# Performance work log

Measured on AMD Instinct MI355X. Metric: run time of the kernel, lower is better.

Reference implementation:

```python
import jax, jax.numpy as jnp
import numpy as np

N_SKILLS = 50000
N_EDGES = 800000
EMB = 128
HEADS = 2
HEAD_DIM = EMB // HEADS  # 64
N_LAYERS = 2
NEG_SLOPE = 0.2  # PyG GATv2Conv default negative_slope


def setup_inputs() -> dict:
    key = jax.random.key(0)
    ks = jax.random.split(key, 10)
    # Random edges with no self loops (PyG remove_self_loops is then a no-op).
    src = jax.random.randint(ks[0], (N_EDGES,), 0, N_SKILLS)
    off = jax.random.randint(ks[1], (N_EDGES,), 1, N_SKILLS)
    dst = (src + off) % N_SKILLS
    edge_index = jnp.stack([src, dst]).astype(jnp.int64)
    edge_weight = jax.random.uniform(ks[2], (N_EDGES,), dtype=jnp.float32)
    scale = 1.0 / np.sqrt(EMB)
    emb = jax.random.normal(ks[3], (N_SKILLS, EMB), dtype=jnp.float32)
    Wl = jax.random.normal(ks[4], (N_LAYERS, EMB, EMB), dtype=jnp.float32) * scale  # lin_l (source)
    Wr = jax.random.normal(ks[5], (N_LAYERS, EMB, EMB), dtype=jnp.float32) * scale  # lin_r (target)
    We = jax.random.normal(ks[6], (N_LAYERS, 1, EMB), dtype=jnp.float32)            # lin_edge
    att = jax.random.normal(ks[7], (N_LAYERS, HEADS, HEAD_DIM), dtype=jnp.float32) * (1.0 / np.sqrt(HEAD_DIM))
    bias = jnp.zeros((N_LAYERS, EMB), dtype=jnp.float32)
    return {"edge_index": edge_index, "edge_weight": edge_weight, "emb": emb,
            "Wl": Wl, "Wr": Wr, "We": We, "att": att, "bias": bias}


def _gatv2_layer(h, src, dst, ew, Wl, Wr, We, att, bias):
    """One GATv2Conv layer (concat heads, add_self_loops with fill_value='mean')."""
    N = h.shape[0]
    xl = (h @ Wl).reshape(N, HEADS, HEAD_DIM)  # source transform
    xr = (h @ Wr).reshape(N, HEADS, HEAD_DIM)  # target transform
    # Self-loop edge attr = mean of incoming edge attrs (PyG fill_value='mean').
    deg = jnp.zeros((N,), h.dtype).at[dst].add(1.0)
    loop_w = jnp.zeros((N,), h.dtype).at[dst].add(ew) / jnp.maximum(deg, 1.0)
    ar = jnp.arange(N)
    srcA = jnp.concatenate([src, ar])
    dstA = jnp.concatenate([dst, ar])
    ewA = jnp.concatenate([ew, loop_w])[:, None]           # [E+N, 1]
    e_emb = (ewA @ We).reshape(-1, HEADS, HEAD_DIM)        # [E+N, H, D]
    msg = xl[srcA]                                         # gathered source feats
    x = jax.nn.leaky_relu(msg + xr[dstA] + e_emb, NEG_SLOPE)
    alpha = jnp.einsum('ehd,hd->eh', x, att)               # [E+N, H]
    # Scatter-softmax over edges grouped by target node.
    amax = jnp.full((N, HEADS), -jnp.inf, h.dtype).at[dstA].max(alpha)
    ex = jnp.exp(alpha - amax[dstA])
    denom = jnp.zeros((N, HEADS), h.dtype).at[dstA].add(ex)
    a = ex / denom[dstA]                                   # denom > 0 (self loops)
    out = jnp.zeros((N, HEADS, HEAD_DIM), h.dtype).at[dstA].add(msg * a[:, :, None])
    return out.reshape(N, EMB) + bias


def reference(edge_index, edge_weight, emb, Wl, Wr, We, att, bias):
    src, dst = edge_index[0], edge_index[1]
    h = emb  # skill_emb(arange(num_skills))
    for l in range(N_LAYERS):
        h = _gatv2_layer(h, src, dst, edge_weight, Wl[l], Wr[l], We[l], att[l], bias[l])
        h = jax.nn.elu(h)  # dropout omitted (eval mode)
    return h
```

## Files before the change

### kernel.cpp

```cpp
#include <hip/hip_runtime.h>
#include <hip/hip_fp16.h>
#include <cstdint>

#define NEG_SLOPE 0.2f
#define MAXDEG 64

typedef __attribute__((ext_vector_type(8))) short bf16x8;
typedef __attribute__((ext_vector_type(4))) float f32x4;
typedef _Float16 h2_t __attribute__((ext_vector_type(2)));

__device__ inline short bf16_rne(float x) {
    uint32_t u = __float_as_uint(x);
    return (short)((u + 0x7FFF + ((u >> 16) & 1)) >> 16);
}
__device__ inline float bf16_to_f32(short s) {
    uint32_t u = ((uint32_t)(uint16_t)s) << 16;
    return __uint_as_float(u);
}
__device__ inline float fdot2(__half2 a, __half2 b, float c) {
    return __builtin_amdgcn_fdot2(*(h2_t*)&a, *(h2_t*)&b, c, false);
}
__device__ inline __half2 hmax2(__half2 a, __half2 b) {
    uint32_t au = *(uint32_t*)&a, bu = *(uint32_t*)&b, du;
    asm("v_pk_max_f16 %0, %1, %2" : "=v"(du) : "v"(au), "v"(bu));
    return *(__half2*)&du;
}
__device__ inline float fma_mix_lo(float e, uint32_t xh, float c) {
    float d;
    asm("v_fma_mix_f32 %0, %1, %2, %3 op_sel_hi:[0,1,0]" : "=v"(d) : "v"(e), "v"(xh), "v"(c));
    return d;
}
__device__ inline float fma_mix_hi(float e, uint32_t xh, float c) {
    float d;
    asm("v_fma_mix_f32 %0, %1, %2, %3 op_sel:[0,1,0] op_sel_hi:[0,1,0]" : "=v"(d) : "v"(e), "v"(xh), "v"(c));
    return d;
}
template <int CTRL, int RMASK, int BMASK, bool BC>
__device__ inline float dpp_add(float v) {
    int t = __builtin_amdgcn_update_dpp(0, __float_as_int(v), CTRL, RMASK, BMASK, BC);
    return v + __int_as_float(t);
}
__device__ inline float red8(float p) {
    p = dpp_add<0xB1, 0xF, 0xF, true>(p);
    p = dpp_add<0x4E, 0xF, 0xF, true>(p);
    int a = __builtin_amdgcn_update_dpp(0, __float_as_int(p), 0x114, 0xF, 0xA, false);
    int b = __builtin_amdgcn_update_dpp(0, __float_as_int(p), 0x104, 0xF, 0x5, false);
    return p + __int_as_float(a) + __int_as_float(b);
}


__global__ __launch_bounds__(256) void k_init(int* __restrict__ cursor, int N) {
    int i = blockIdx.x * 256 + threadIdx.x;
    if (i < N) cursor[i] = i * MAXDEG;
}

__global__ __launch_bounds__(256) void k_fillb(const int* __restrict__ ei, const float* __restrict__ ew,
                                               int* __restrict__ cursor, int2* __restrict__ bucket, int E) {
    int i0 = (blockIdx.x * 256 + threadIdx.x) * 8;
    if (i0 >= E) return;
    if (i0 + 7 < E) {
        int4 sa = *(const int4*)&ei[i0];
        int4 sb = *(const int4*)&ei[i0 + 4];
        int4 da = *(const int4*)&ei[E + i0];
        int4 db = *(const int4*)&ei[E + i0 + 4];
        float4 wa = *(const float4*)&ew[i0];
        float4 wb = *(const float4*)&ew[i0 + 4];
        int p0 = atomicAdd(&cursor[da.x], 1);
        int p1 = atomicAdd(&cursor[da.y], 1);
        int p2 = atomicAdd(&cursor[da.z], 1);
        int p3 = atomicAdd(&cursor[da.w], 1);
        int p4 = atomicAdd(&cursor[db.x], 1);
        int p5 = atomicAdd(&cursor[db.y], 1);
        int p6 = atomicAdd(&cursor[db.z], 1);
        int p7 = atomicAdd(&cursor[db.w], 1);
        bucket[p0] = make_int2(sa.x, __float_as_int(wa.x));
        bucket[p1] = make_int2(sa.y, __float_as_int(wa.y));
        bucket[p2] = make_int2(sa.z, __float_as_int(wa.z));
        bucket[p3] = make_int2(sa.w, __float_as_int(wa.w));
        bucket[p4] = make_int2(sb.x, __float_as_int(wb.x));
        bucket[p5] = make_int2(sb.y, __float_as_int(wb.y));
        bucket[p6] = make_int2(sb.z, __float_as_int(wb.z));
        bucket[p7] = make_int2(sb.w, __float_as_int(wb.w));
    } else {
        for (int i = i0; i < E; ++i) {
            int pos = atomicAdd(&cursor[ei[E + i]], 1);
            bucket[pos] = make_int2(ei[i], __float_as_int(ew[i]));
        }
    }
}

__global__ __launch_bounds__(256) void k_cvtW(const float* __restrict__ Wl, const float* __restrict__ Wr,
                                              short* __restrict__ wt) {
    int b = blockIdx.x;
    int l = b >> 1, mat = b & 1;
    const float* W = (mat ? Wr : Wl) + (size_t)l * 16384;
    short* dst = wt + (size_t)b * 40960;
    int t = threadIdx.x;
    int n = t >> 1, half = t & 1;
    for (int chunk = 0; chunk < 4; ++chunk) {
        short hi16[16], lo16[16];
#pragma unroll
        for (int i = 0; i < 16; ++i) {
            int kk = half * 16 + i;
            float x = W[(size_t)(chunk * 32 + kk) * 128 + n];
            short h = bf16_rne(x);
            float r = x - bf16_to_f32(h);
            hi16[i] = h;
            lo16[i] = bf16_rne(r);
        }
        short* base = dst + chunk * 10240;
#pragma unroll
        for (int i = 0; i < 16; ++i) {
            base[n * 40 + half * 16 + i] = hi16[i];
            base[5120 + n * 40 + half * 16 + i] = lo16[i];
        }
    }
}

__global__ __launch_bounds__(256) void k_gemm_mfma(const float* __restrict__ H, const short* __restrict__ wt,
                                                   __half* __restrict__ Olh, float* __restrict__ Or, int N) {
    __shared__ __align__(16) short smem[2560 + 2560 + 10240];
    short* Ahi = smem;
    short* Alo = smem + 2560;
    short* Wst = smem + 5120;
    const short* wtm = wt + (size_t)blockIdx.y * 40960;
    int t = threadIdx.x;
    int w = t >> 6, lane = t & 63;
    int m = lane & 15, g = lane >> 4;
    int r0 = blockIdx.x * 64;
    f32x4 acc[8];
#pragma unroll
    for (int i = 0; i < 8; ++i) acc[i] = (f32x4){0.f, 0.f, 0.f, 0.f};

    int rr = t >> 2, q = t & 3;
    for (int chunk = 0; chunk < 4; ++chunk) {
        const short* wsrc = wtm + chunk * 10240;
#pragma unroll
        for (int i = 0; i < 5; ++i) {
            int u = t + i * 256;
            *(int4*)&Wst[u * 8] = *(const int4*)&wsrc[u * 8];
        }
        {
            int r = r0 + rr;
            float v[8];
            if (r < N) {
                float4 a = *(const float4*)&H[(size_t)r * 128 + chunk * 32 + q * 8];
                float4 b = *(const float4*)&H[(size_t)r * 128 + chunk * 32 + q * 8 + 4];
                v[0] = a.x; v[1] = a.y; v[2] = a.z; v[3] = a.w;
                v[4] = b.x; v[5] = b.y; v[6] = b.z; v[7] = b.w;
            } else {
#pragma unroll
                for (int i = 0; i < 8; ++i) v[i] = 0.f;
            }
            short hi8[8], lo8[8];
#pragma unroll
            for (int i = 0; i < 8; ++i) {
                short h = bf16_rne(v[i]);
                hi8[i] = h;
                lo8[i] = bf16_rne(v[i] - bf16_to_f32(h));
            }
            *(int4*)&Ahi[rr * 40 + q * 8] = *(int4*)hi8;
            *(int4*)&Alo[rr * 40 + q * 8] = *(int4*)lo8;
        }
        __syncthreads();
        bf16x8 ahi = *(bf16x8*)&Ahi[(w * 16 + m) * 40 + g * 8];
        bf16x8 alo = *(bf16x8*)&Alo[(w * 16 + m) * 40 + g * 8];
#pragma unroll
        for (int nf = 0; nf < 8; ++nf) {
            bf16x8 bhi = *(bf16x8*)&Wst[(nf * 16 + m) * 40 + g * 8];
            bf16x8 blo = *(bf16x8*)&Wst[5120 + (nf * 16 + m) * 40 + g * 8];
            acc[nf] = __builtin_amdgcn_mfma_f32_16x16x32_bf16(ahi, bhi, acc[nf], 0, 0, 0);
            acc[nf] = __builtin_amdgcn_mfma_f32_16x16x32_bf16(alo, bhi, acc[nf], 0, 0, 0);
            acc[nf] = __builtin_amdgcn_mfma_f32_16x16x32_bf16(ahi, blo, acc[nf], 0, 0, 0);
        }
        __syncthreads();
    }
    if (blockIdx.y == 0) {
#pragma unroll
        for (int nf = 0; nf < 8; ++nf)
#pragma unroll
            for (int j = 0; j < 4; ++j) {
                int row = r0 + w * 16 + g * 4 + j;
                if (row < N) Olh[(size_t)row * 128 + nf * 16 + m] = __float2half_rn(acc[nf][j]);
            }
    } else {
#pragma unroll
        for (int nf = 0; nf < 8; ++nf)
#pragma unroll
            for (int j = 0; j < 4; ++j) {
                int row = r0 + w * 16 + g * 4 + j;
                if (row < N) Or[(size_t)row * 128 + nf * 16 + m] = acc[nf][j];
            }
    }
}


#define STAGE(IT, R0, R1, W0, W1, V0, V1)                                      \
    {                                                                          \
        int slot0 = (IT) * 8 + e4;                                             \
        int slot1 = slot0 + 4;                                                 \
        int s0i = __builtin_amdgcn_ds_bpermute(slot0 << 2, recAll.x);          \
        int w0i = __builtin_amdgcn_ds_bpermute(slot0 << 2, recAll.y);          \
        int s1i = __builtin_amdgcn_ds_bpermute(slot1 << 2, recAll.x);          \
        int w1i = __builtin_amdgcn_ds_bpermute(slot1 << 2, recAll.y);          \
        V0 = slot0 < deg; V1 = slot1 < deg;                                    \
        int off0 = ((V0 ? s0i : n) << 7) + d0;                                 \
        int off1 = ((V1 ? s1i : n) << 7) + d0;                                 \
        W0 = V0 ? __int_as_float(w0i) : 0.f;                                   \
        W1 = V1 ? __int_as_float(w1i) : 0.f;                                   \
        R0 = *(const int4*)(xl + off0);                                        \
        R1 = *(const int4*)(xl + off1);                                        \
    }

#define CONSUME(R0, R1, W0, W1, V0, V1)                                        \
    {                                                                          \
        __half2* x0h = (__half2*)&(R0);                                        \
        __half2* x1h = (__half2*)&(R1);                                        \
        uint32_t* x0u = (uint32_t*)&(R0);                                      \
        uint32_t* x1u = (uint32_t*)&(R1);                                      \
        __half2 w0h = __half2half2(__float2half_rn(W0));                       \
        __half2 w1h = __half2half2(__float2half_rn(W1));                       \
        float p0 = 0.f, p1 = 0.f;                                              \
        _Pragma("unroll")                                                      \
        for (int i = 0; i < 4; ++i) {                                          \
            __half2 t0 = __hfma2(w0h, weh[i], __hadd2(x0h[i], xrh[i]));        \
            __half2 t1 = __hfma2(w1h, weh[i], __hadd2(x1h[i], xrh[i]));        \
            t0 = hmax2(t0, __hmul2(t0, sl2));                                  \
            t1 = hmax2(t1, __hmul2(t1, sl2));                                  \
            p0 = fdot2(t0, ath[i], p0);                                        \
            p1 = fdot2(t1, ath[i], p1);                                        \
        }                                                                      \
        p0 = red8(p0);                                                         \
        p1 = red8(p1);                                                         \
        float e0 = exp2f(p0);                                                  \
        float e1 = exp2f(p1);                                                  \
        e0 = V0 ? e0 : 0.f;                                                    \
        e1 = V1 ? e1 : 0.f;                                                    \
        den += e0 + e1;                                                        \
        wacc += W0 + W1;                                                       \
        _Pragma("unroll")                                                      \
        for (int i = 0; i < 4; ++i) {                                          \
            a[2*i]   = fma_mix_lo(e0, x0u[i], a[2*i]);                         \
            a[2*i+1] = fma_mix_hi(e0, x0u[i], a[2*i+1]);                       \
            a[2*i]   = fma_mix_lo(e1, x1u[i], a[2*i]);                         \
            a[2*i+1] = fma_mix_hi(e1, x1u[i], a[2*i+1]);                       \
        }                                                                      \
    }

__global__ __launch_bounds__(256) void k_node(const __half* __restrict__ xl, const float* __restrict__ xr,
                                              const int* __restrict__ cursor, const int2* __restrict__ bucket,
                                              const float* __restrict__ We, const float* __restrict__ att,
                                              const float* __restrict__ bias, float* __restrict__ out, int N) {
    int wid = threadIdx.x >> 6;
    int lane = threadIdx.x & 63;
    int n = blockIdx.x * 4 + wid;
    if (n >= N) return;
    int sub = lane & 15, e4 = lane >> 4;
    int d0 = sub * 8;
    const float LOG2E = 1.44269504f;
    __half2 weh[4], ath[4], xrh[4];
    {
        float4 weA = *(const float4*)(We + d0),  weB = *(const float4*)(We + d0 + 4);
        float4 atA = *(const float4*)(att + d0), atB = *(const float4*)(att + d0 + 4);
        const float* xrp = xr + n * 128 + d0;
        float4 xrA = *(const float4*)xrp, xrB = *(const float4*)(xrp + 4);
        weh[0] = __floats2half2_rn(weA.x, weA.y); weh[1] = __floats2half2_rn(weA.z, weA.w);
        weh[2] = __floats2half2_rn(weB.x, weB.y); weh[3] = __floats2half2_rn(weB.z, weB.w);
        ath[0] = __floats2half2_rn(atA.x * LOG2E, atA.y * LOG2E);
        ath[1] = __floats2half2_rn(atA.z * LOG2E, atA.w * LOG2E);
        ath[2] = __floats2half2_rn(atB.x * LOG2E, atB.y * LOG2E);
        ath[3] = __floats2half2_rn(atB.z * LOG2E, atB.w * LOG2E);
        xrh[0] = __floats2half2_rn(xrA.x, xrA.y); xrh[1] = __floats2half2_rn(xrA.z, xrA.w);
        xrh[2] = __floats2half2_rn(xrB.x, xrB.y); xrh[3] = __floats2half2_rn(xrB.z, xrB.w);
    }
    __half2 sl2 = __half2half2(__float2half_rn(NEG_SLOPE));
    int beg = n * MAXDEG;
    int deg = cursor[n] - beg;
    int iters = (deg + 7) >> 3;
    int2 recAll = bucket[beg + lane];
    float den = 0.f, wacc = 0.f;
    float a[8] = {};

    int4 pR0, pR1; float pW0, pW1; bool pV0, pV1;
    int4 qR0, qR1; float qW0, qW1; bool qV0, qV1;
    STAGE(0, pR0, pR1, pW0, pW1, pV0, pV1);
    for (int it = 0; it < iters; ) {
        if (it + 1 < iters) STAGE(it + 1, qR0, qR1, qW0, qW1, qV0, qV1);
        CONSUME(pR0, pR1, pW0, pW1, pV0, pV1);
        ++it;
        if (it >= iters) break;
        if (it + 1 < iters) STAGE(it + 1, pR0, pR1, pW0, pW1, pV0, pV1);
        CONSUME(qR0, qR1, qW0, qW1, qV0, qV1);
        ++it;
    }
#pragma unroll
    for (int off = 16; off <= 32; off <<= 1) {
        den += __shfl_xor(den, off);
        wacc += __shfl_xor(wacc, off);
#pragma unroll
        for (int i = 0; i < 8; ++i) a[i] += __shfl_xor(a[i], off);
    }
    {
        float lw = wacc / (float)max(deg, 1);
        int4 rawn = *(const int4*)(xl + (n << 7) + d0);
        __half2* xh = (__half2*)&rawn;
        uint32_t* xu = (uint32_t*)&rawn;
        __half2 lwh = __half2half2(__float2half_rn(lw));
        float p = 0.f;
#pragma unroll
        for (int i = 0; i < 4; ++i) {
            __half2 t = __hfma2(lwh, weh[i], __hadd2(xh[i], xrh[i]));
            t = hmax2(t, __hmul2(t, sl2));
            p = fdot2(t, ath[i], p);
        }
        p = red8(p);
        float e = exp2f(p);
        den += e;
#pragma unroll
        for (int i = 0; i < 4; ++i) {
            a[2*i]   = fma_mix_lo(e, xu[i], a[2*i]);
            a[2*i+1] = fma_mix_hi(e, xu[i], a[2*i+1]);
        }
    }
    float inv = 1.f / den;
    float4 biA = *(const float4*)(bias + d0), biB = *(const float4*)(bias + d0 + 4);
    float o[8];
    o[0] = a[0] * inv + biA.x; o[1] = a[1] * inv + biA.y;
    o[2] = a[2] * inv + biA.z; o[3] = a[3] * inv + biA.w;
    o[4] = a[4] * inv + biB.x; o[5] = a[5] * inv + biB.y;
    o[6] = a[6] * inv + biB.z; o[7] = a[7] * inv + biB.w;
#pragma unroll
    for (int i = 0; i < 8; ++i)
        o[i] = o[i] > 0.f ? o[i] : exp2f(o[i] * LOG2E) - 1.f;
    if (e4 == 0) {
        float* op = out + n * 128 + d0;
        *(float4*)op       = make_float4(o[0], o[1], o[2], o[3]);
        *(float4*)(op + 4) = make_float4(o[4], o[5], o[6], o[7]);
    }
}


extern "C" void kernel_launch(void* const* d_in, const int* in_sizes, int n_in,
                              void* d_out, int out_size, void* d_ws, size_t ws_size,
                              hipStream_t stream) {
    const int*   ei   = (const int*)d_in[0];
    const float* ew   = (const float*)d_in[1];
    const float* emb  = (const float*)d_in[2];
    const float* Wl   = (const float*)d_in[3];
    const float* Wr   = (const float*)d_in[4];
    const float* We   = (const float*)d_in[5];
    const float* att  = (const float*)d_in[6];
    const float* bias = (const float*)d_in[7];
    int E = in_sizes[1];
    int N = in_sizes[2] / 128;

    char* p = (char*)d_ws;
    auto alloc = [&](size_t bytes) { char* r = p; p += (bytes + 255) & ~(size_t)255; return r; };
    __half* xl    = (__half*)alloc((size_t)N * 128 * 2);
    float*  xr    = (float*)alloc((size_t)N * 128 * 4);
    int2*   bucket= (int2*)alloc(((size_t)N * MAXDEG + 64) * 8);
    int*    cursor= (int*)alloc((size_t)N * 4);
    short*  wtbuf = (short*)alloc((size_t)4 * 40960 * 2);
    if ((size_t)(p - (char*)d_ws) > ws_size) return;

    int ib = (N + 255) / 256;
    int fb = (E / 8 + 255) / 256;
    k_init<<<ib, 256, 0, stream>>>(cursor, N);
    k_fillb<<<fb, 256, 0, stream>>>(ei, ew, cursor, bucket, E);
    k_cvtW<<<4, 256, 0, stream>>>(Wl, Wr, wtbuf);

    int gb = (N + 63) / 64;
    int nb = (N + 3) / 4;
    const float* h = emb;
    for (int l = 0; l < 2; ++l) {
        float* outl = (float*)d_out;
        k_gemm_mfma<<<dim3(gb, 2), 256, 0, stream>>>(h, wtbuf + (size_t)l * 81920, xl, xr, N);
        k_node<<<nb, 256, 0, stream>>>(xl, xr, cursor, bucket,
                                       We + (size_t)l * 128, att + (size_t)l * 128,
                                       bias + (size_t)l * 128, outl, N);
        h = outl;
    }
}
```

Baseline: 204.6 us.

## Store xr in fp16, prescale source indices, batch four gathers per lane

The target-side projection xr is now written in fp16 by the GEMM, which halves its write and read traffic and removes the float-to-half conversion in the node kernel. Bucket entries store the source index pre-shifted to a byte offset, saving address arithmetic per edge. The node loop drops the two-stage software pipeline and instead issues four independent gathers per lane per iteration over sixteen edges, aiming for more memory-level parallelism at the cost of explicit prefetch across iterations. The fp16 xr adds a small amount of rounding error.

```diff
diff --git a/kernel.cpp b/kernel.cpp
--- a/kernel.cpp
+++ b/kernel.cpp
@@ -73,18 +73,18 @@
         int p5 = atomicAdd(&cursor[db.y], 1);
         int p6 = atomicAdd(&cursor[db.z], 1);
         int p7 = atomicAdd(&cursor[db.w], 1);
-        bucket[p0] = make_int2(sa.x, __float_as_int(wa.x));
-        bucket[p1] = make_int2(sa.y, __float_as_int(wa.y));
-        bucket[p2] = make_int2(sa.z, __float_as_int(wa.z));
-        bucket[p3] = make_int2(sa.w, __float_as_int(wa.w));
-        bucket[p4] = make_int2(sb.x, __float_as_int(wb.x));
-        bucket[p5] = make_int2(sb.y, __float_as_int(wb.y));
-        bucket[p6] = make_int2(sb.z, __float_as_int(wb.z));
-        bucket[p7] = make_int2(sb.w, __float_as_int(wb.w));
+        bucket[p0] = make_int2(sa.x << 8, __float_as_int(wa.x));
+        bucket[p1] = make_int2(sa.y << 8, __float_as_int(wa.y));
+        bucket[p2] = make_int2(sa.z << 8, __float_as_int(wa.z));
+        bucket[p3] = make_int2(sa.w << 8, __float_as_int(wa.w));
+        bucket[p4] = make_int2(sb.x << 8, __float_as_int(wb.x));
+        bucket[p5] = make_int2(sb.y << 8, __float_as_int(wb.y));
+        bucket[p6] = make_int2(sb.z << 8, __float_as_int(wb.z));
+        bucket[p7] = make_int2(sb.w << 8, __float_as_int(wb.w));
     } else {
         for (int i = i0; i < E; ++i) {
             int pos = atomicAdd(&cursor[ei[E + i]], 1);
-            bucket[pos] = make_int2(ei[i], __float_as_int(ew[i]));
+            bucket[pos] = make_int2(ei[i] << 8, __float_as_int(ew[i]));
         }
     }
 }
@@ -118,12 +118,13 @@
 }
 
 __global__ __launch_bounds__(256) void k_gemm_mfma(const float* __restrict__ H, const short* __restrict__ wt,
-                                                   __half* __restrict__ Olh, float* __restrict__ Or, int N) {
+                                                   __half* __restrict__ Olh, __half* __restrict__ Orh, int N) {
     __shared__ __align__(16) short smem[2560 + 2560 + 10240];
     short* Ahi = smem;
     short* Alo = smem + 2560;
     short* Wst = smem + 5120;
     const short* wtm = wt + (size_t)blockIdx.y * 40960;
+    __half* O = blockIdx.y ? Orh : Olh;
     int t = threadIdx.x;
     int w = t >> 6, lane = t & 63;
     int m = lane & 15, g = lane >> 4;
@@ -175,79 +176,17 @@
         }
         __syncthreads();
     }
-    if (blockIdx.y == 0) {
-#pragma unroll
-        for (int nf = 0; nf < 8; ++nf)
-#pragma unroll
-            for (int j = 0; j < 4; ++j) {
-                int row = r0 + w * 16 + g * 4 + j;
-                if (row < N) Olh[(size_t)row * 128 + nf * 16 + m] = __float2half_rn(acc[nf][j]);
-            }
-    } else {
-#pragma unroll
-        for (int nf = 0; nf < 8; ++nf)
-#pragma unroll
-            for (int j = 0; j < 4; ++j) {
-                int row = r0 + w * 16 + g * 4 + j;
-                if (row < N) Or[(size_t)row * 128 + nf * 16 + m] = acc[nf][j];
-            }
-    }
-}
-
-
-#define STAGE(IT, R0, R1, W0, W1, V0, V1)                                      \
-    {                                                                          \
-        int slot0 = (IT) * 8 + e4;                                             \
-        int slot1 = slot0 + 4;                                                 \
-        int s0i = __builtin_amdgcn_ds_bpermute(slot0 << 2, recAll.x);          \
-        int w0i = __builtin_amdgcn_ds_bpermute(slot0 << 2, recAll.y);          \
-        int s1i = __builtin_amdgcn_ds_bpermute(slot1 << 2, recAll.x);          \
-        int w1i = __builtin_amdgcn_ds_bpermute(slot1 << 2, recAll.y);          \
-        V0 = slot0 < deg; V1 = slot1 < deg;                                    \
-        int off0 = ((V0 ? s0i : n) << 7) + d0;                                 \
-        int off1 = ((V1 ? s1i : n) << 7) + d0;                                 \
-        W0 = V0 ? __int_as_float(w0i) : 0.f;                                   \
-        W1 = V1 ? __int_as_float(w1i) : 0.f;                                   \
-        R0 = *(const int4*)(xl + off0);                                        \
-        R1 = *(const int4*)(xl + off1);                                        \
-    }
-
-#define CONSUME(R0, R1, W0, W1, V0, V1)                                        \
-    {                                                                          \
-        __half2* x0h = (__half2*)&(R0);                                        \
-        __half2* x1h = (__half2*)&(R1);                                        \
-        uint32_t* x0u = (uint32_t*)&(R0);                                      \
-        uint32_t* x1u = (uint32_t*)&(R1);                                      \
-        __half2 w0h = __half2half2(__float2half_rn(W0));                       \
-        __half2 w1h = __half2half2(__float2half_rn(W1));                       \
-        float p0 = 0.f, p1 = 0.f;                                              \
-        _Pragma("unroll")                                                      \
-        for (int i = 0; i < 4; ++i) {                                          \
-            __half2 t0 = __hfma2(w0h, weh[i], __hadd2(x0h[i], xrh[i]));        \
-            __half2 t1 = __hfma2(w1h, weh[i], __hadd2(x1h[i], xrh[i]));        \
-            t0 = hmax2(t0, __hmul2(t0, sl2));                                  \
-            t1 = hmax2(t1, __hmul2(t1, sl2));                                  \
-            p0 = fdot2(t0, ath[i], p0);                                        \
-            p1 = fdot2(t1, ath[i], p1);                                        \
-        }                                                                      \
-        p0 = red8(p0);                                                         \
-        p1 = red8(p1);                                                         \
-        float e0 = exp2f(p0);                                                  \
-        float e1 = exp2f(p1);                                                  \
-        e0 = V0 ? e0 : 0.f;                                                    \
-        e1 = V1 ? e1 : 0.f;                                                    \
-        den += e0 + e1;                                                        \
-        wacc += W0 + W1;                                                       \
-        _Pragma("unroll")                                                      \
-        for (int i = 0; i < 4; ++i) {                                          \
-            a[2*i]   = fma_mix_lo(e0, x0u[i], a[2*i]);                         \
-            a[2*i+1] = fma_mix_hi(e0, x0u[i], a[2*i+1]);                       \
-            a[2*i]   = fma_mix_lo(e1, x1u[i], a[2*i]);                         \
-            a[2*i+1] = fma_mix_hi(e1, x1u[i], a[2*i+1]);                       \
-        }                                                                      \
-    }
-
-__global__ __launch_bounds__(256) void k_node(const __half* __restrict__ xl, const float* __restrict__ xr,
+#pragma unroll
+    for (int nf = 0; nf < 8; ++nf)
+#pragma unroll
+        for (int j = 0; j < 4; ++j) {
+            int row = r0 + w * 16 + g * 4 + j;
+            if (row < N) O[(size_t)row * 128 + nf * 16 + m] = __float2half_rn(acc[nf][j]);
+        }
+}
+
+
+__global__ __launch_bounds__(256) void k_node(const __half* __restrict__ xl, const __half* __restrict__ xr_h,
                                               const int* __restrict__ cursor, const int2* __restrict__ bucket,
                                               const float* __restrict__ We, const float* __restrict__ att,
                                               const float* __restrict__ bias, float* __restrict__ out, int N) {
@@ -257,41 +196,68 @@
     if (n >= N) return;
     int sub = lane & 15, e4 = lane >> 4;
     int d0 = sub * 8;
+    int d02 = d0 * 2;
+    int nOff = n << 8;
+    const char* xlb = (const char*)xl;
     const float LOG2E = 1.44269504f;
-    __half2 weh[4], ath[4], xrh[4];
+    __half2 weh[4], ath[4], xrv[4];
     {
         float4 weA = *(const float4*)(We + d0),  weB = *(const float4*)(We + d0 + 4);
         float4 atA = *(const float4*)(att + d0), atB = *(const float4*)(att + d0 + 4);
-        const float* xrp = xr + n * 128 + d0;
-        float4 xrA = *(const float4*)xrp, xrB = *(const float4*)(xrp + 4);
         weh[0] = __floats2half2_rn(weA.x, weA.y); weh[1] = __floats2half2_rn(weA.z, weA.w);
         weh[2] = __floats2half2_rn(weB.x, weB.y); weh[3] = __floats2half2_rn(weB.z, weB.w);
         ath[0] = __floats2half2_rn(atA.x * LOG2E, atA.y * LOG2E);
         ath[1] = __floats2half2_rn(atA.z * LOG2E, atA.w * LOG2E);
         ath[2] = __floats2half2_rn(atB.x * LOG2E, atB.y * LOG2E);
         ath[3] = __floats2half2_rn(atB.z * LOG2E, atB.w * LOG2E);
-        xrh[0] = __floats2half2_rn(xrA.x, xrA.y); xrh[1] = __floats2half2_rn(xrA.z, xrA.w);
-        xrh[2] = __floats2half2_rn(xrB.x, xrB.y); xrh[3] = __floats2half2_rn(xrB.z, xrB.w);
+        int4 xrr = *(const int4*)((const char*)xr_h + nOff + d02);
+        __half2* xp = (__half2*)&xrr;
+        xrv[0] = xp[0]; xrv[1] = xp[1]; xrv[2] = xp[2]; xrv[3] = xp[3];
     }
     __half2 sl2 = __half2half2(__float2half_rn(NEG_SLOPE));
     int beg = n * MAXDEG;
     int deg = cursor[n] - beg;
-    int iters = (deg + 7) >> 3;
+    int iters = (deg + 15) >> 4;
     int2 recAll = bucket[beg + lane];
     float den = 0.f, wacc = 0.f;
     float a[8] = {};
 
-    int4 pR0, pR1; float pW0, pW1; bool pV0, pV1;
-    int4 qR0, qR1; float qW0, qW1; bool qV0, qV1;
-    STAGE(0, pR0, pR1, pW0, pW1, pV0, pV1);
-    for (int it = 0; it < iters; ) {
-        if (it + 1 < iters) STAGE(it + 1, qR0, qR1, qW0, qW1, qV0, qV1);
-        CONSUME(pR0, pR1, pW0, pW1, pV0, pV1);
-        ++it;
-        if (it >= iters) break;
-        if (it + 1 < iters) STAGE(it + 1, pR0, pR1, pW0, pW1, pV0, pV1);
-        CONSUME(qR0, qR1, qW0, qW1, qV0, qV1);
-        ++it;
+    for (int it = 0; it < iters; ++it) {
+        int slotb = it * 16 + e4 * 4;
+        int4 R[4]; float Wv[4]; bool V[4];
+#pragma unroll
+        for (int j = 0; j < 4; ++j) {
+            int slot = slotb + j;
+            int si = __builtin_amdgcn_ds_bpermute(slot << 2, recAll.x);
+            int wi = __builtin_amdgcn_ds_bpermute(slot << 2, recAll.y);
+            V[j] = slot < deg;
+            int off = (V[j] ? si : nOff) + d02;
+            Wv[j] = V[j] ? __int_as_float(wi) : 0.f;
+            R[j] = *(const int4*)(xlb + off);
+        }
+#pragma unroll
+        for (int j = 0; j < 4; ++j) {
+            __half2* xh = (__half2*)&R[j];
+            uint32_t* xu = (uint32_t*)&R[j];
+            __half2 wh = __half2half2(__float2half_rn(Wv[j]));
+            float p = 0.f;
+#pragma unroll
+            for (int i = 0; i < 4; ++i) {
+                __half2 t = __hfma2(wh, weh[i], __hadd2(xh[i], xrv[i]));
+                t = hmax2(t, __hmul2(t, sl2));
+                p = fdot2(t, ath[i], p);
+            }
+            p = red8(p);
+            float e = exp2f(p);
+            e = V[j] ? e : 0.f;
+            den += e;
+            wacc += Wv[j];
+#pragma unroll
+            for (int i = 0; i < 4; ++i) {
+                a[2*i]   = fma_mix_lo(e, xu[i], a[2*i]);
+                a[2*i+1] = fma_mix_hi(e, xu[i], a[2*i+1]);
+            }
+        }
     }
 #pragma unroll
     for (int off = 16; off <= 32; off <<= 1) {
@@ -302,14 +268,14 @@
     }
     {
         float lw = wacc / (float)max(deg, 1);
-        int4 rawn = *(const int4*)(xl + (n << 7) + d0);
+        int4 rawn = *(const int4*)(xlb + nOff + d02);
         __half2* xh = (__half2*)&rawn;
         uint32_t* xu = (uint32_t*)&rawn;
         __half2 lwh = __half2half2(__float2half_rn(lw));
         float p = 0.f;
 #pragma unroll
         for (int i = 0; i < 4; ++i) {
-            __half2 t = __hfma2(lwh, weh[i], __hadd2(xh[i], xrh[i]));
+            __half2 t = __hfma2(lwh, weh[i], __hadd2(xh[i], xrv[i]));
             t = hmax2(t, __hmul2(t, sl2));
             p = fdot2(t, ath[i], p);
         }
@@ -357,7 +323,7 @@
     char* p = (char*)d_ws;
     auto alloc = [&](size_t bytes) { char* r = p; p += (bytes + 255) & ~(size_t)255; return r; };
     __half* xl    = (__half*)alloc((size_t)N * 128 * 2);
-    float*  xr    = (float*)alloc((size_t)N * 128 * 4);
+    __half* xr    = (__half*)alloc((size_t)N * 128 * 2);
     int2*   bucket= (int2*)alloc(((size_t)N * MAXDEG + 64) * 8);
     int*    cursor= (int*)alloc((size_t)N * 4);
     short*  wtbuf = (short*)alloc((size_t)4 * 40960 * 2);
```

New measurement: 211.2 us. 1.03x slower.
